# Kernel optimization log

Hardware: AMD Instinct MI355X
Metric: run time of the kernel (lower is better)

Reference implementation:

```python
import jax, jax.numpy as jnp
import numpy as np

N = 100000
E = 1600000
F_IN = 128
H1, C1 = 8, 8          # conv1: heads=8, hidden_channels=8 -> concat dim 64
H2, C2 = 1, 40         # conv2: heads=1, out=num_classes=40, concat=False
NEG_SLOPE = 0.2
EPS = 1e-16


def setup_inputs() -> dict:
    key = jax.random.key(0)
    ks = jax.random.split(key, 10)
    x = jax.random.normal(ks[0], (N, F_IN), dtype=jnp.float32)
    edge_index = jax.random.randint(ks[1], (2, E), 0, N, dtype=jnp.int32)
    s1 = 1.0 / np.sqrt(F_IN)
    s2 = 1.0 / np.sqrt(H1 * C1)
    W1 = jax.random.normal(ks[2], (F_IN, H1 * C1), dtype=jnp.float32) * s1
    att_src1 = jax.random.normal(ks[3], (H1, C1), dtype=jnp.float32) * s2
    att_dst1 = jax.random.normal(ks[4], (H1, C1), dtype=jnp.float32) * s2
    b1 = jnp.zeros((H1 * C1,), dtype=jnp.float32)
    W2 = jax.random.normal(ks[5], (H1 * C1, H2 * C2), dtype=jnp.float32) * s2
    att_src2 = jax.random.normal(ks[6], (H2, C2), dtype=jnp.float32) * (1.0 / np.sqrt(C2))
    att_dst2 = jax.random.normal(ks[7], (H2, C2), dtype=jnp.float32) * (1.0 / np.sqrt(C2))
    b2 = jnp.zeros((C2,), dtype=jnpp_zeros_dtype()) if False else jnp.zeros((C2,), dtype=jnp.float32)
    return {"x": x, "W1": W1, "att_src1": att_src1, "att_dst1": att_dst1, "b1": b1,
            "W2": W2, "att_src2": att_src2, "att_dst2": att_dst2, "b2": b2,
            "edge_index": edge_index}


def _gat_conv(x, W, att_src, att_dst, bias, src, dst, num_nodes, concat):
    """PyG GATConv (eval mode, self-loops already added to src/dst)."""
    H, C = att_src.shape
    h = (x @ W).reshape(num_nodes, H, C)                 # [N, H, C]
    a_src = jnp.sum(h * att_src[None], axis=-1)          # [N, H]
    a_dst = jnp.sum(h * att_dst[None], axis=-1)          # [N, H]
    e = a_src[src] + a_dst[dst]                          # [Etot, H]
    e = jax.nn.leaky_relu(e, NEG_SLOPE)
    # segment softmax over incoming edges of each dst node
    e_max = jax.ops.segment_max(e, dst, num_segments=num_nodes)   # [N, H]
    ex = jnp.exp(e - e_max[dst])
    denom = jax.ops.segment_sum(ex, dst, num_segments=num_nodes)  # [N, H]
    alpha = ex / (denom[dst] + EPS)                      # [Etot, H]
    msg = h[src] * alpha[..., None]                      # [Etot, H, C]
    out = jax.ops.segment_sum(msg, dst, num_segments=num_nodes)   # [N, H, C]
    if concat:
        out = out.reshape(num_nodes, H * C)
    else:
        out = out.mean(axis=1)
    return out + bias


def reference(x, W1, att_src1, att_dst1, b1, W2, att_src2, att_dst2, b2, edge_index):
    # add self-loops (PyG GATConv default add_self_loops=True)
    loops = jnp.arange(N, dtype=edge_index.dtype)
    src = jnp.concatenate([edge_index[0], loops])
    dst = jnp.concatenate([edge_index[1], loops])
    # dropout layers are identity in eval mode
    emb = jax.nn.elu(_gat_conv(x, W1, att_src1, att_dst1, b1, src, dst, N, True))
    logits = _gat_conv(emb, W2, att_src2, att_dst2, b2, src, dst, N, False)
    return jax.nn.log_softmax(logits, axis=1), emb


def jnp_zeros_dtype():
    return jnp.float32
```

## Files before the change

kernel.cpp:

```cpp
#include <hip/hip_runtime.h>
#include <hip/hip_fp16.h>
#include <math.h>

#define NN 100000
#define EE 1600000
#define ET (EE + NN)
#define FIN 128
#define D1 64
#define H1 8
#define C1 8
#define C2 40
#define NEG 0.2f
#define EPSV 1e-16f
#define LOG2E 1.4426950408889634f

#define NBKT 391
#define BCAPP 6784
#define EBUF 5120
#define CHUNK 2048
#define NBB ((ET + CHUNK - 1) / CHUNK)
#define G1B ((NN + 63) / 64)
#define PREPB 16
#define DB 32
#define DSTR 32

typedef _Float16 f16x8 __attribute__((ext_vector_type(8)));
typedef float f32x4 __attribute__((ext_vector_type(4)));

__device__ __forceinline__ void edge_sd(int e, const int* __restrict__ ei, int& s, int& d) {
  if (e < EE) { s = ei[e]; d = ei[EE + e]; }
  else        { s = e - EE; d = s; }
}

__global__ __launch_bounds__(256) void k1_kernel(
    const int* __restrict__ ei, int* __restrict__ gcur, int* __restrict__ ecsr,
    const float* __restrict__ W1, const float* __restrict__ as1, const float* __restrict__ ad1,
    const float* __restrict__ W2, const float* __restrict__ as2, const float* __restrict__ ad2w,
    __half* __restrict__ Wf1, __half* __restrict__ Wf2) {
  __shared__ int lh[NBKT], lres[NBKT], lcur[NBKT];
  int t = threadIdx.x;
  if (blockIdx.x < NBB) {
    for (int i = t; i < NBKT; i += 256) { lh[i] = 0; lcur[i] = 0; }
    __syncthreads();
    int e0 = blockIdx.x * CHUNK;
    int e1 = min(e0 + CHUNK, ET);
    for (int e = e0 + t; e < e1; e += 256) {
      int d = (e < EE) ? ei[EE + e] : e - EE;
      atomicAdd(&lh[d >> 8], 1);
    }
    __syncthreads();
    for (int i = t; i < NBKT; i += 256)
      if (lh[i]) lres[i] = atomicAdd(&gcur[i], lh[i]);
    __syncthreads();
    for (int e = e0 + t; e < e1; e += 256) {
      int s, d; edge_sd(e, ei, s, d);
      int b = d >> 8;
      int lp = atomicAdd(&lcur[b], 1);
      ecsr[b * BCAPP + lres[b] + lp] = s | ((d & 255) << 17);
    }
  } else {
    int gid = (blockIdx.x - NBB) * 256 + t;
    int stride = PREPB * 256;
    for (int idx = gid; idx < 4 * 5 * 64 * 8; idx += stride) {
      int j = idx & 7, l = (idx >> 3) & 63;
      int g = idx >> 9;
      int ct = g % 5, kk = g / 5;
      int kdim = kk * 32 + (l >> 4) * 8 + j;
      int c = l & 15;
      float v;
      if (ct < 4) v = W1[kdim * 64 + ct * 16 + c];
      else {
        const float* aw = (c < 8) ? as1 : ad1;
        int hh = c & 7;
        float acc = 0.f;
        for (int q = 0; q < 8; ++q) acc += W1[kdim * 64 + hh * 8 + q] * aw[hh * 8 + q];
        v = acc * LOG2E;
      }
      Wf1[idx] = __float2half(v);
    }
    for (int idx = gid; idx < 2 * 3 * 64 * 8; idx += stride) {
      int j = idx & 7, l = (idx >> 3) & 63;
      int g = idx >> 9;
      int ct = g % 3, kk = g / 3;
      int kdim = kk * 32 + (l >> 4) * 8 + j;
      int c = ct * 16 + (l & 15);
      float v = 0.f;
      if (c < C2) v = W2[kdim * C2 + c];
      else if (c == 40 || c == 41) {
        const float* aw = (c == 40) ? as2 : ad2w;
        float acc = 0.f;
        for (int q = 0; q < C2; ++q) acc += W2[kdim * C2 + q] * aw[q];
        v = acc * LOG2E;
      }
      Wf2[idx] = __float2half(v);
    }
  }
}

__global__ __launch_bounds__(256) void k2_kernel(
    const int* __restrict__ gcur, int2* __restrict__ rowrng, int* __restrict__ ecsr,
    int* __restrict__ dhist,
    const float* __restrict__ x, const __half* __restrict__ Wf1,
    __half* __restrict__ h, __half* __restrict__ as_h, float* __restrict__ ad) {
  __shared__ int ebuf[EBUF];
  __shared__ int hist[256];
  __shared__ int sd[256];
  __shared__ int ldh[DB];
  int t = threadIdx.x;
  if (blockIdx.x < NBKT) {
    int b = blockIdx.x;
    int base = b * BCAPP;
    int cnt = gcur[b];
    hist[t] = 0;
    if (t < DB) ldh[t] = 0;
    __syncthreads();
    for (int i = t; i < cnt; i += 256) {
      int p = ecsr[base + i];
      ebuf[i] = p;
      atomicAdd(&hist[p >> 17], 1);
    }
    __syncthreads();
    int h0 = hist[t];
    int p8 = (h0 + 7) & ~7;
    sd[t] = p8;
    __syncthreads();
    for (int off = 1; off < 256; off <<= 1) {
      int xv = sd[t];
      int yv = (t >= off) ? sd[t - off] : 0;
      __syncthreads();
      sd[t] = xv + yv;
      __syncthreads();
    }
    int runp = sd[t] - p8;
    int g = b * 256 + t;
    if (g < NN) {
      rowrng[g] = make_int2(base + runp, base + runp + h0);
      atomicAdd(&ldh[min(h0 >> 3, DB - 1)], 1);
    }
    hist[t] = runp;
    __syncthreads();
    if (t < DB && ldh[t]) atomicAdd(&dhist[t * DSTR], ldh[t]);
    for (int i = t; i < cnt; i += 256) {
      int p = ebuf[i];
      int pos = atomicAdd(&hist[p >> 17], 1);
      ecsr[base + pos] = p & 0x1FFFF;
    }
    __syncthreads();
    if (g < NN && h0 < p8) {
      int first = ecsr[base + runp];
      for (int q = runp + h0; q < runp + p8; ++q) ecsr[base + q] = first;
    }
  } else {
    int blk = blockIdx.x - NBKT;
    int w = t >> 6, lane = t & 63;
    int col = lane & 15, kg = lane >> 4;
    int node0 = blk * 64 + w * 16;
    int nodeA = min(node0 + col, NN - 1);
    const float* xr = x + (size_t)nodeA * FIN + kg * 8;
    const f16x8* Wq = (const f16x8*)Wf1;
    f32x4 acc0 = {0.f,0.f,0.f,0.f}, acc1 = acc0, acc2 = acc0, acc3 = acc0, acc4 = acc0;
#pragma unroll
    for (int kk = 0; kk < 4; ++kk) {
      float4 xa = *(const float4*)(xr + kk * 32);
      float4 xb = *(const float4*)(xr + kk * 32 + 4);
      f16x8 a;
      a[0] = (_Float16)xa.x; a[1] = (_Float16)xa.y; a[2] = (_Float16)xa.z; a[3] = (_Float16)xa.w;
      a[4] = (_Float16)xb.x; a[5] = (_Float16)xb.y; a[6] = (_Float16)xb.z; a[7] = (_Float16)xb.w;
      acc0 = __builtin_amdgcn_mfma_f32_16x16x32_f16(a, Wq[(kk * 5 + 0) * 64 + lane], acc0, 0, 0, 0);
      acc1 = __builtin_amdgcn_mfma_f32_16x16x32_f16(a, Wq[(kk * 5 + 1) * 64 + lane], acc1, 0, 0, 0);
      acc2 = __builtin_amdgcn_mfma_f32_16x16x32_f16(a, Wq[(kk * 5 + 2) * 64 + lane], acc2, 0, 0, 0);
      acc3 = __builtin_amdgcn_mfma_f32_16x16x32_f16(a, Wq[(kk * 5 + 3) * 64 + lane], acc3, 0, 0, 0);
      acc4 = __builtin_amdgcn_mfma_f32_16x16x32_f16(a, Wq[(kk * 5 + 4) * 64 + lane], acc4, 0, 0, 0);
    }
#pragma unroll
    for (int reg = 0; reg < 4; ++reg) {
      int nr = node0 + kg * 4 + reg;
      if (nr < NN) {
        h[(size_t)nr * 64 +  0 + col] = __float2half(acc0[reg]);
        h[(size_t)nr * 64 + 16 + col] = __float2half(acc1[reg]);
        h[(size_t)nr * 64 + 32 + col] = __float2half(acc2[reg]);
        h[(size_t)nr * 64 + 48 + col] = __float2half(acc3[reg]);
        float v = acc4[reg];
        if (col < 8) as_h[nr * 8 + col] = __float2half(v);
        else         ad[nr * 8 + col - 8] = v;
      }
    }
  }
}

__global__ __launch_bounds__(256) void k3_kernel(
    const int2* __restrict__ rowrng, const int* __restrict__ dhist,
    int* __restrict__ dcur, int* __restrict__ perm) {
  __shared__ int lh[DB], lres[DB], lcur[DB], pbase[DB];
  int t = threadIdx.x;
  if (t < DB) { lh[t] = 0; lcur[t] = 0; }
  __syncthreads();
  int n = blockIdx.x * 256 + t;
  int bkt = 0;
  if (n < NN) {
    int2 rr = rowrng[n];
    bkt = min((rr.y - rr.x) >> 3, DB - 1);
    atomicAdd(&lh[bkt], 1);
  }
  __syncthreads();
  if (t == 0) {
    int acc = 0;
    for (int q = 0; q < DB; ++q) { pbase[q] = acc; acc += dhist[q * DSTR]; }
  }
  if (t < DB && lh[t]) lres[t] = atomicAdd(&dcur[t * DSTR], lh[t]);
  __syncthreads();
  if (n < NN) {
    int lp = atomicAdd(&lcur[bkt], 1);
    perm[pbase[bkt] + lres[bkt] + lp] = n;
  }
}

#define CONS(u, avh, valid) do { \
    float xx = __half2float(avh) + adv; xx = fmaxf(xx, NEG * xx); \
    float e = (valid) ? exp2f(xx) : 0.f; den += e; \
    float2 f; \
    f = __half22float2(*(const __half2*)&(u).x); a0 = fmaf(f.x, e, a0); a1 = fmaf(f.y, e, a1); \
    f = __half22float2(*(const __half2*)&(u).y); a2 = fmaf(f.x, e, a2); a3 = fmaf(f.y, e, a3); \
    f = __half22float2(*(const __half2*)&(u).z); a4 = fmaf(f.x, e, a4); a5 = fmaf(f.y, e, a5); \
    f = __half22float2(*(const __half2*)&(u).w); a6 = fmaf(f.x, e, a6); a7 = fmaf(f.y, e, a7); \
  } while (0)

#define ISSUE1(OFF, U, V) do { \
    int4 c0_ = *(const int4*)&csr[beg + (OFF)]; \
    int4 c1_ = *(const int4*)&csr[beg + (OFF) + 4]; \
    int sj_[8] = {c0_.x, c0_.y, c0_.z, c0_.w, c1_.x, c1_.y, c1_.z, c1_.w}; \
    _Pragma("unroll") \
    for (int r_ = 0; r_ < 8; ++r_) { \
      U[r_] = *(const uint4*)(h + ((size_t)(uint)sj_[r_] << 6) + (k << 3)); \
      V[r_] = as_h[(uint)sj_[r_] * 8u + k]; \
    } \
  } while (0)

__global__ __launch_bounds__(256) void agg1_kernel(
    const int* __restrict__ perm,
    const int2* __restrict__ rowrng, const int* __restrict__ csr,
    const __half* __restrict__ as_h, const float* __restrict__ ad,
    const __half* __restrict__ h, const float* __restrict__ b1,
    float* __restrict__ emb) {
  int t = threadIdx.x;
  int lane = t & 63;
  int o = lane >> 3, k = lane & 7;
  int node = perm[blockIdx.x * 32 + (t >> 6) * 8 + o];
  int2 rr = rowrng[node];
  int beg = rr.x, deg = rr.y - rr.x;
  float adv = ad[node * 8 + k];
  float den = 0.f;
  float a0=0.f,a1=0.f,a2=0.f,a3=0.f,a4=0.f,a5=0.f,a6=0.f,a7=0.f;
  uint4 uA[8]; __half vA[8];
  ISSUE1(0, uA, vA);
  for (int i = 0; i < deg; i += 16) {
    uint4 uB[8]; __half vB[8];
    bool haveB = (i + 8 < deg);
    if (haveB) ISSUE1(i + 8, uB, vB);
#pragma unroll
    for (int r = 0; r < 8; ++r) CONS(uA[r], vA[r], i + r < deg);
    if (i + 16 < deg) ISSUE1(i + 16, uA, vA);
    if (haveB) {
#pragma unroll
      for (int r = 0; r < 8; ++r) CONS(uB[r], vB[r], i + 8 + r < deg);
    }
  }
  float4 bv0 = ((const float4*)b1)[2 * k];
  float4 bv1 = ((const float4*)b1)[2 * k + 1];
  float inv = 1.0f / (den + EPSV);
  float v0 = fmaf(a0, inv, bv0.x), v1 = fmaf(a1, inv, bv0.y);
  float v2 = fmaf(a2, inv, bv0.z), v3 = fmaf(a3, inv, bv0.w);
  float v4 = fmaf(a4, inv, bv1.x), v5 = fmaf(a5, inv, bv1.y);
  float v6 = fmaf(a6, inv, bv1.z), v7 = fmaf(a7, inv, bv1.w);
  v0 = v0 > 0.f ? v0 : expm1f(v0); v1 = v1 > 0.f ? v1 : expm1f(v1);
  v2 = v2 > 0.f ? v2 : expm1f(v2); v3 = v3 > 0.f ? v3 : expm1f(v3);
  v4 = v4 > 0.f ? v4 : expm1f(v4); v5 = v5 > 0.f ? v5 : expm1f(v5);
  v6 = v6 > 0.f ? v6 : expm1f(v6); v7 = v7 > 0.f ? v7 : expm1f(v7);
  float4 s0; s0.x = v0; s0.y = v1; s0.z = v2; s0.w = v3;
  float4 s1; s1.x = v4; s1.y = v5; s1.z = v6; s1.w = v7;
  float* ep = emb + (size_t)node * D1 + (k << 3);
  ((float4*)ep)[0] = s0; ((float4*)ep)[1] = s1;
}

__global__ __launch_bounds__(256) void gemm2_kernel(
    const float* __restrict__ emb, const __half* __restrict__ Wf2,
    __half* __restrict__ h2, float* __restrict__ ad2) {
  int t = threadIdx.x;
  int w = t >> 6, lane = t & 63;
  int col = lane & 15, kg = lane >> 4;
  int node0 = blockIdx.x * 64 + w * 16;
  int nodeA = min(node0 + col, NN - 1);
  const float* er = emb + (size_t)nodeA * D1 + kg * 8;
  const f16x8* Wq = (const f16x8*)Wf2;
  f32x4 acc0 = {0.f,0.f,0.f,0.f}, acc1 = acc0, acc2 = acc0;
#pragma unroll
  for (int kk = 0; kk < 2; ++kk) {
    float4 xa = *(const float4*)(er + kk * 32);
    float4 xb = *(const float4*)(er + kk * 32 + 4);
    f16x8 a;
    a[0] = (_Float16)xa.x; a[1] = (_Float16)xa.y; a[2] = (_Float16)xa.z; a[3] = (_Float16)xa.w;
    a[4] = (_Float16)xb.x; a[5] = (_Float16)xb.y; a[6] = (_Float16)xb.z; a[7] = (_Float16)xb.w;
    acc0 = __builtin_amdgcn_mfma_f32_16x16x32_f16(a, Wq[(kk * 3 + 0) * 64 + lane], acc0, 0, 0, 0);
    acc1 = __builtin_amdgcn_mfma_f32_16x16x32_f16(a, Wq[(kk * 3 + 1) * 64 + lane], acc1, 0, 0, 0);
    acc2 = __builtin_amdgcn_mfma_f32_16x16x32_f16(a, Wq[(kk * 3 + 2) * 64 + lane], acc2, 0, 0, 0);
  }
#pragma unroll
  for (int reg = 0; reg < 4; ++reg) {
    int nr = node0 + kg * 4 + reg;
    if (nr < NN) {
      h2[(size_t)nr * 64 +  0 + col] = __float2half(acc0[reg]);
      h2[(size_t)nr * 64 + 16 + col] = __float2half(acc1[reg]);
      float v = acc2[reg];
      if (col < 8)       h2[(size_t)nr * 64 + 32 + col] = __float2half(v);
      else if (col == 8) h2[(size_t)nr * 64 + 40] = __float2half(v);
      else if (col == 9) ad2[nr] = v;
    }
  }
}

#define ISSUE2(OFF, U, V) do { \
    int4 c0_ = *(const int4*)&csr[beg + (OFF)]; \
    int4 c1_ = *(const int4*)&csr[beg + (OFF) + 4]; \
    int sj_[8] = {c0_.x, c0_.y, c0_.z, c0_.w, c1_.x, c1_.y, c1_.z, c1_.w}; \
    _Pragma("unroll") \
    for (int r_ = 0; r_ < 8; ++r_) { \
      const __half* rp_ = h2 + ((size_t)(uint)sj_[r_] << 6); \
      U[r_] = *(const uint4*)(rp_ + (kc << 3)); \
      V[r_] = rp_[40]; \
    } \
  } while (0)

__global__ __launch_bounds__(256) void agg2_kernel(
    const int* __restrict__ perm,
    const int2* __restrict__ rowrng, const int* __restrict__ csr,
    const float* __restrict__ ad, const __half* __restrict__ h2,
    const float* __restrict__ b2, float* __restrict__ out) {
  int t = threadIdx.x;
  int lane = t & 63;
  int o = lane >> 3, k = lane & 7;
  int kc = min(k, 4);
  int node = perm[blockIdx.x * 32 + (t >> 6) * 8 + o];
  int2 rr = rowrng[node];
  int beg = rr.x, deg = rr.y - rr.x;
  float adv = ad[node];
  float den = 0.f;
  float a0=0.f,a1=0.f,a2=0.f,a3=0.f,a4=0.f,a5=0.f,a6=0.f,a7=0.f;
  uint4 uA[8]; __half vA[8];
  ISSUE2(0, uA, vA);
  for (int i = 0; i < deg; i += 16) {
    uint4 uB[8]; __half vB[8];
    bool haveB = (i + 8 < deg);
    if (haveB) ISSUE2(i + 8, uB, vB);
#pragma unroll
    for (int r = 0; r < 8; ++r) CONS(uA[r], vA[r], i + r < deg);
    if (i + 16 < deg) ISSUE2(i + 16, uA, vA);
    if (haveB) {
#pragma unroll
      for (int r = 0; r < 8; ++r) CONS(uB[r], vB[r], i + 8 + r < deg);
    }
  }
  float4 bv0 = ((const float4*)b2)[2 * kc];
  float4 bv1 = ((const float4*)b2)[2 * kc + 1];
  float inv = 1.0f / (den + EPSV);
  float v0 = fmaf(a0, inv, bv0.x), v1 = fmaf(a1, inv, bv0.y);
  float v2 = fmaf(a2, inv, bv0.z), v3 = fmaf(a3, inv, bv0.w);
  float v4 = fmaf(a4, inv, bv1.x), v5 = fmaf(a5, inv, bv1.y);
  float v6 = fmaf(a6, inv, bv1.z), v7 = fmaf(a7, inv, bv1.w);
  bool act = (k < 5);
  float m = act ? fmaxf(fmaxf(fmaxf(v0, v1), fmaxf(v2, v3)),
                        fmaxf(fmaxf(v4, v5), fmaxf(v6, v7))) : -INFINITY;
#pragma unroll
  for (int off = 1; off < 8; off <<= 1) m = fmaxf(m, __shfl_xor(m, off, 64));
  float ex = act ? (__expf(v0 - m) + __expf(v1 - m) + __expf(v2 - m) + __expf(v3 - m) +
                    __expf(v4 - m) + __expf(v5 - m) + __expf(v6 - m) + __expf(v7 - m)) : 0.f;
#pragma unroll
  for (int off = 1; off < 8; off <<= 1) ex += __shfl_xor(ex, off, 64);
  if (act) {
    float lls = m + logf(ex);
    float4 s0; s0.x = v0 - lls; s0.y = v1 - lls; s0.z = v2 - lls; s0.w = v3 - lls;
    float4 s1; s1.x = v4 - lls; s1.y = v5 - lls; s1.z = v6 - lls; s1.w = v7 - lls;
    float* op = out + (size_t)node * C2 + (k << 3);
    ((float4*)op)[0] = s0; ((float4*)op)[1] = s1;
  }
}

extern "C" void kernel_launch(void* const* d_in, const int* in_sizes, int n_in,
                              void* d_out, int out_size, void* d_ws, size_t ws_size,
                              hipStream_t stream) {
  const float* x    = (const float*)d_in[0];
  const float* W1   = (const float*)d_in[1];
  const float* as1w = (const float*)d_in[2];
  const float* ad1w = (const float*)d_in[3];
  const float* b1   = (const float*)d_in[4];
  const float* W2   = (const float*)d_in[5];
  const float* as2w = (const float*)d_in[6];
  const float* ad2w = (const float*)d_in[7];
  const float* b2   = (const float*)d_in[8];
  const int*   ei   = (const int*)d_in[9];

  float* out   = (float*)d_out;
  float* outls = out;
  float* emb   = out + (long)NN * C2;

  char* wsb = (char*)d_ws;
  __half* h1   = (__half*)wsb; wsb += sizeof(__half) * (size_t)NN * D1;
  __half* h2   = (__half*)wsb; wsb += sizeof(__half) * ((size_t)NN * 64 + 64);
  __half* ash1 = (__half*)wsb; wsb += sizeof(__half) * (size_t)NN * H1;
  float* adst1 = (float*)wsb; wsb += sizeof(float) * (size_t)NN * H1;
  float* adst2 = (float*)wsb; wsb += sizeof(float) * (size_t)NN;
  int2* rowrng = (int2*)wsb;  wsb += sizeof(int2) * (size_t)NN;
  int* perm    = (int*)wsb;   wsb += sizeof(int) * (size_t)NN;
  int* gcur    = (int*)wsb;   wsb += sizeof(int) * (NBKT + 4);
  int* dhist   = (int*)wsb;   wsb += sizeof(int) * DB * DSTR;
  int* dcur    = (int*)wsb;   wsb += sizeof(int) * DB * DSTR;
  __half* Wf1  = (__half*)wsb; wsb += sizeof(__half) * 4 * 5 * 64 * 8;
  __half* Wf2  = (__half*)wsb; wsb += sizeof(__half) * 2 * 3 * 64 * 8;
  int* ecsr    = (int*)wsb;   wsb += sizeof(int) * (size_t)NBKT * BCAPP;

  hipMemsetAsync(gcur, 0, sizeof(int) * (NBKT + 4 + 2 * DB * DSTR), stream);
  k1_kernel<<<NBB + PREPB, 256, 0, stream>>>(ei, gcur, ecsr,
                                             W1, as1w, ad1w, W2, as2w, ad2w, Wf1, Wf2);
  k2_kernel<<<NBKT + G1B, 256, 0, stream>>>(gcur, rowrng, ecsr, dhist,
                                            x, Wf1, h1, ash1, adst1);
  k3_kernel<<<(NN + 255) / 256, 256, 0, stream>>>(rowrng, dhist, dcur, perm);
  agg1_kernel<<<NN / 32, 256, 0, stream>>>(perm, rowrng, ecsr, ash1, adst1, h1, b1, emb);
  gemm2_kernel<<<(NN + 63) / 64, 256, 0, stream>>>(emb, Wf2, h2, adst2);
  agg2_kernel<<<NN / 32, 256, 0, stream>>>(perm, rowrng, ecsr, adst2, h2, b2, outls);
}
```

Measured before the change: 261.9 us.

## Share attention-logit loads across lanes via shuffles and drop CSR padding fill

```diff
diff --git a/kernel.cpp b/kernel.cpp
--- a/kernel.cpp
+++ b/kernel.cpp
@@ -145,11 +145,6 @@
       int pos = atomicAdd(&hist[p >> 17], 1);
       ecsr[base + pos] = p & 0x1FFFF;
     }
-    __syncthreads();
-    if (g < NN && h0 < p8) {
-      int first = ecsr[base + runp];
-      for (int q = runp + h0; q < runp + p8; ++q) ecsr[base + q] = first;
-    }
   } else {
     int blk = blockIdx.x - NBKT;
     int w = t >> 6, lane = t & 63;
@@ -205,7 +200,7 @@
   __syncthreads();
   if (t == 0) {
     int acc = 0;
-    for (int q = 0; q < DB; ++q) { pbase[q] = acc; acc += dhist[q * DSTR]; }
+    for (int q = DB - 1; q >= 0; --q) { pbase[q] = acc; acc += dhist[q * DSTR]; }
   }
   if (t < DB && lh[t]) lres[t] = atomicAdd(&dcur[t * DSTR], lh[t]);
   __syncthreads();
@@ -214,27 +209,6 @@
     perm[pbase[bkt] + lres[bkt] + lp] = n;
   }
 }
-
-#define CONS(u, avh, valid) do { \
-    float xx = __half2float(avh) + adv; xx = fmaxf(xx, NEG * xx); \
-    float e = (valid) ? exp2f(xx) : 0.f; den += e; \
-    float2 f; \
-    f = __half22float2(*(const __half2*)&(u).x); a0 = fmaf(f.x, e, a0); a1 = fmaf(f.y, e, a1); \
-    f = __half22float2(*(const __half2*)&(u).y); a2 = fmaf(f.x, e, a2); a3 = fmaf(f.y, e, a3); \
-    f = __half22float2(*(const __half2*)&(u).z); a4 = fmaf(f.x, e, a4); a5 = fmaf(f.y, e, a5); \
-    f = __half22float2(*(const __half2*)&(u).w); a6 = fmaf(f.x, e, a6); a7 = fmaf(f.y, e, a7); \
-  } while (0)
-
-#define ISSUE1(OFF, U, V) do { \
-    int4 c0_ = *(const int4*)&csr[beg + (OFF)]; \
-    int4 c1_ = *(const int4*)&csr[beg + (OFF) + 4]; \
-    int sj_[8] = {c0_.x, c0_.y, c0_.z, c0_.w, c1_.x, c1_.y, c1_.z, c1_.w}; \
-    _Pragma("unroll") \
-    for (int r_ = 0; r_ < 8; ++r_) { \
-      U[r_] = *(const uint4*)(h + ((size_t)(uint)sj_[r_] << 6) + (k << 3)); \
-      V[r_] = as_h[(uint)sj_[r_] * 8u + k]; \
-    } \
-  } while (0)
 
 __global__ __launch_bounds__(256) void agg1_kernel(
     const int* __restrict__ perm,
@@ -244,25 +218,49 @@
     float* __restrict__ emb) {
   int t = threadIdx.x;
   int lane = t & 63;
-  int o = lane >> 3, k = lane & 7;
+  int o = lane >> 3, k = lane & 7, ob = lane & 56;
   int node = perm[blockIdx.x * 32 + (t >> 6) * 8 + o];
   int2 rr = rowrng[node];
   int beg = rr.x, deg = rr.y - rr.x;
   float adv = ad[node * 8 + k];
   float den = 0.f;
   float a0=0.f,a1=0.f,a2=0.f,a3=0.f,a4=0.f,a5=0.f,a6=0.f,a7=0.f;
-  uint4 uA[8]; __half vA[8];
-  ISSUE1(0, uA, vA);
-  for (int i = 0; i < deg; i += 16) {
-    uint4 uB[8]; __half vB[8];
-    bool haveB = (i + 8 < deg);
-    if (haveB) ISSUE1(i + 8, uB, vB);
-#pragma unroll
-    for (int r = 0; r < 8; ++r) CONS(uA[r], vA[r], i + r < deg);
-    if (i + 16 < deg) ISSUE1(i + 16, uA, vA);
-    if (haveB) {
-#pragma unroll
-      for (int r = 0; r < 8; ++r) CONS(uB[r], vB[r], i + 8 + r < deg);
+  for (int i = 0; i < deg; i += 8) {
+    int4 c0 = *(const int4*)&csr[beg + i];
+    int4 c1 = *(const int4*)&csr[beg + i + 4];
+    int sj[8] = {c0.x, c0.y, c0.z, c0.w, c1.x, c1.y, c1.z, c1.w};
+    uint4 u[8];
+#pragma unroll
+    for (int r = 0; r < 8; ++r)
+      if (i + r < deg)
+        u[r] = *(const uint4*)(h + ((size_t)(uint)sj[r] << 6) + (k << 3));
+    uint4 asr = make_uint4(0u, 0u, 0u, 0u);
+    if (i + k < deg)
+      asr = *(const uint4*)(as_h + (size_t)(uint)sj[k] * 8u);
+#pragma unroll
+    for (int r = 0; r < 8; ++r) {
+      if (i + r < deg) {
+        int w0 = __shfl((int)asr.x, ob + r, 64);
+        int w1 = __shfl((int)asr.y, ob + r, 64);
+        int w2 = __shfl((int)asr.z, ob + r, 64);
+        int w3 = __shfl((int)asr.w, ob + r, 64);
+        int wsel = (k & 4) ? ((k & 2) ? w3 : w2) : ((k & 2) ? w1 : w0);
+        uint hb = (k & 1) ? ((uint)wsel >> 16) : ((uint)wsel & 0xFFFFu);
+        float av = __half2float(__ushort_as_half((unsigned short)hb));
+        float xx = av + adv;
+        xx = fmaxf(xx, NEG * xx);
+        float e = exp2f(xx);
+        den += e;
+        const __half* hp = (const __half*)&u[r];
+        a0 = fmaf(__half2float(hp[0]), e, a0);
+        a1 = fmaf(__half2float(hp[1]), e, a1);
+        a2 = fmaf(__half2float(hp[2]), e, a2);
+        a3 = fmaf(__half2float(hp[3]), e, a3);
+        a4 = fmaf(__half2float(hp[4]), e, a4);
+        a5 = fmaf(__half2float(hp[5]), e, a5);
+        a6 = fmaf(__half2float(hp[6]), e, a6);
+        a7 = fmaf(__half2float(hp[7]), e, a7);
+      }
     }
   }
   float4 bv0 = ((const float4*)b1)[2 * k];
@@ -318,18 +316,6 @@
   }
 }
 
-#define ISSUE2(OFF, U, V) do { \
-    int4 c0_ = *(const int4*)&csr[beg + (OFF)]; \
-    int4 c1_ = *(const int4*)&csr[beg + (OFF) + 4]; \
-    int sj_[8] = {c0_.x, c0_.y, c0_.z, c0_.w, c1_.x, c1_.y, c1_.z, c1_.w}; \
-    _Pragma("unroll") \
-    for (int r_ = 0; r_ < 8; ++r_) { \
-      const __half* rp_ = h2 + ((size_t)(uint)sj_[r_] << 6); \
-      U[r_] = *(const uint4*)(rp_ + (kc << 3)); \
-      V[r_] = rp_[40]; \
-    } \
-  } while (0)
-
 __global__ __launch_bounds__(256) void agg2_kernel(
     const int* __restrict__ perm,
     const int2* __restrict__ rowrng, const int* __restrict__ csr,
@@ -337,7 +323,7 @@
     const float* __restrict__ b2, float* __restrict__ out) {
   int t = threadIdx.x;
   int lane = t & 63;
-  int o = lane >> 3, k = lane & 7;
+  int o = lane >> 3, k = lane & 7, ob = lane & 56;
   int kc = min(k, 4);
   int node = perm[blockIdx.x * 32 + (t >> 6) * 8 + o];
   int2 rr = rowrng[node];
@@ -345,18 +331,37 @@
   float adv = ad[node];
   float den = 0.f;
   float a0=0.f,a1=0.f,a2=0.f,a3=0.f,a4=0.f,a5=0.f,a6=0.f,a7=0.f;
-  uint4 uA[8]; __half vA[8];
-  ISSUE2(0, uA, vA);
-  for (int i = 0; i < deg; i += 16) {
-    uint4 uB[8]; __half vB[8];
-    bool haveB = (i + 8 < deg);
-    if (haveB) ISSUE2(i + 8, uB, vB);
-#pragma unroll
-    for (int r = 0; r < 8; ++r) CONS(uA[r], vA[r], i + r < deg);
-    if (i + 16 < deg) ISSUE2(i + 16, uA, vA);
-    if (haveB) {
-#pragma unroll
-      for (int r = 0; r < 8; ++r) CONS(uB[r], vB[r], i + 8 + r < deg);
+  for (int i = 0; i < deg; i += 8) {
+    int4 c0 = *(const int4*)&csr[beg + i];
+    int4 c1 = *(const int4*)&csr[beg + i + 4];
+    int sj[8] = {c0.x, c0.y, c0.z, c0.w, c1.x, c1.y, c1.z, c1.w};
+    uint4 u[8];
+#pragma unroll
+    for (int r = 0; r < 8; ++r)
+      if (k < 5 && i + r < deg)
+        u[r] = *(const uint4*)(h2 + ((size_t)(uint)sj[r] << 6) + (kc << 3));
+    int attr = 0;
+    if (i + k < deg)
+      attr = (int)*(const unsigned short*)(h2 + ((size_t)(uint)sj[k] << 6) + 40);
+#pragma unroll
+    for (int r = 0; r < 8; ++r) {
+      if (i + r < deg) {
+        int wa = __shfl(attr, ob + r, 64);
+        float av = __half2float(__ushort_as_half((unsigned short)wa));
+        float xx = av + adv;
+        xx = fmaxf(xx, NEG * xx);
+        float e = exp2f(xx);
+        den += e;
+        const __half* hp = (const __half*)&u[r];
+        a0 = fmaf(__half2float(hp[0]), e, a0);
+        a1 = fmaf(__half2float(hp[1]), e, a1);
+        a2 = fmaf(__half2float(hp[2]), e, a2);
+        a3 = fmaf(__half2float(hp[3]), e, a3);
+        a4 = fmaf(__half2float(hp[4]), e, a4);
+        a5 = fmaf(__half2float(hp[5]), e, a5);
+        a6 = fmaf(__half2float(hp[6]), e, a6);
+        a7 = fmaf(__half2float(hp[7]), e, a7);
+      }
     }
   }
   float4 bv0 = ((const float4*)b2)[2 * kc];
```

Result: slower. 273.8 us (+4.5%).
